# Kernel optimization log

Hardware: AMD Instinct MI355X
Metric: run time of the kernel (lower is better)

The kernel has to match this reference:

```python
import jax, jax.numpy as jnp
import numpy as np

EPS = 1e-8
LRELU_SLOPE = 0.2
ACT_GAIN = float(np.sqrt(2.0))  # def_gain for lrelu
GAIN = 1.0                      # forward default
CLAMP = 256.0


def setup_inputs() -> dict:
    key = jax.random.key(0)
    k1, k2 = jax.random.split(key)
    x = jax.random.normal(k1, (8, 128, 32, 32, 32), dtype=jnp.float32)
    weight = jax.random.normal(k2, (128, 128, 3, 3, 3), dtype=jnp.float32)
    bias = jnp.zeros((128,), dtype=jnp.float32)
    return {"x": x, "weight": weight, "bias": bias}


def _modulated_conv3d(x, weight, styles, padding, demodulate=True):
    # x: [B, Cin, D, H, W], weight: [Cout, Cin, kd, kh, kw], styles: [B, Cin]
    w = weight[None] * styles[:, None, :, None, None, None]  # [B, Cout, Cin, kd, kh, kw]
    if demodulate:
        dcoefs = jax.lax.rsqrt(jnp.sum(jnp.square(w), axis=(2, 3, 4, 5)) + EPS)  # [B, Cout]
        w = w * dcoefs[:, :, None, None, None, None]
    pad = [(padding, padding)] * 3

    def per_sample(xi, wi):
        # xi: [Cin, D, H, W], wi: [Cout, Cin, kd, kh, kw]
        return jax.lax.conv_general_dilated(
            xi[None], wi, window_strides=(1, 1, 1), padding=pad,
            dimension_numbers=("NCDHW", "OIDHW", "NCDHW"))[0]

    return jax.vmap(per_sample)(x, w)  # [B, Cout, D, H, W]


def reference(x, weight, bias):
    padding = weight.shape[-1] // 2
    styles = jnp.ones((x.shape[0], weight.shape[1]), dtype=x.dtype)
    y = _modulated_conv3d(x, weight, styles, padding)
    y = jax.nn.leaky_relu(y + bias[None, :, None, None, None], LRELU_SLOPE)
    # clamp_gain(act, act_gain*gain, 256*gain)
    return jnp.clip(y * (ACT_GAIN * GAIN), -CLAMP * GAIN, CLAMP * GAIN)
```

## Files before the change

kernel.cpp:

```cpp
#include <hip/hip_runtime.h>

typedef short bf16x8 __attribute__((ext_vector_type(8)));
typedef float f32x4  __attribute__((ext_vector_type(4)));

static __device__ __forceinline__ unsigned short f2bf(float f) {
    unsigned int u = __builtin_bit_cast(unsigned int, f);
    u += 0x7FFFu + ((u >> 16) & 1u);
    return (unsigned short)(u >> 16);
}

__global__ __launch_bounds__(256) void prep_w_k(const float* __restrict__ w,
                                                unsigned short* __restrict__ wn) {
    const int co = blockIdx.x;
    const int t  = threadIdx.x;
    const float* wc = w + co * 3456;
    float s = 0.f;
    for (int i = t; i < 3456; i += 256) { float v = wc[i]; s += v * v; }
#pragma unroll
    for (int off = 32; off; off >>= 1) s += __shfl_down(s, off);
    __shared__ float red[4];
    __shared__ float dsh;
    if ((t & 63) == 0) red[t >> 6] = s;
    __syncthreads();
    if (t == 0) dsh = rsqrtf(red[0] + red[1] + red[2] + red[3] + 1e-8f);
    __syncthreads();
    const float d = dsh;
    for (int i = t; i < 3456; i += 256) {
        int ci = i / 27, tap = i - ci * 27;
        float v = wc[i] * d;
        wn[((tap * 4 + (ci >> 5)) * 128 + co) * 32 + (ci & 31)] = f2bf(v);
    }
}

#define XSBASE 1280
__global__ __launch_bounds__(512, 2) void conv3d_k(
    const float* __restrict__ x, const unsigned short* __restrict__ wn,
    const float* __restrict__ bias, float* __restrict__ out) {
    __shared__ __align__(16) unsigned short lds[59200];

    const int t    = threadIdx.x;
    const int lane = t & 63;
    const int wid  = t >> 6;
    const int wr   = wid >> 1;
    const int wcn  = wid & 1;
    const int ll   = lane & 15;
    const int g    = lane >> 4;

    const int bid = blockIdx.x;
    const int b  = bid >> 6;
    const int dt = (bid >> 3) & 7, ht = bid & 7;
    const int d0 = dt * 4, h0 = ht * 4;

    const int sw  = t & 31;
    const int sg  = (t >> 5) & 3;
    const int rhi = t >> 7;
    const int bco = t >> 2, bgb = t & 3;

    f32x4 acc[8][4];
#pragma unroll
    for (int i = 0; i < 8; ++i)
#pragma unroll
        for (int j = 0; j < 4; ++j) acc[i][j] = (f32x4){0.f, 0.f, 0.f, 0.f};

    float bv[4][4];
#pragma unroll
    for (int nf = 0; nf < 4; ++nf) {
        f32x4 bb = *(const f32x4*)&bias[wcn * 64 + nf * 16 + g * 4];
#pragma unroll
        for (int q = 0; q < 4; ++q) bv[nf][q] = bb[q];
    }

    if (t < 288) {
        int pi  = t >> 2;
        int row = pi >> 1;
        int pos = row * 34 + (pi & 1) * 33;
        bf16x8 z = {0, 0, 0, 0, 0, 0, 0, 0};
        *(bf16x8*)&lds[(XSBASE + pos * 5 + (t & 3)) * 8] = z;
    }

    for (int c = 0; c < 4; ++c) {
        const int cibase = c * 32;
#pragma unroll
        for (int p = 0; p < 9; ++p) {
            int rowid = p * 4 + rhi;
            int pd = (rowid * 43) >> 8;
            int ph = rowid - pd * 6;
            int d = d0 - 1 + pd, h = h0 - 1 + ph;
            bool ok = ((unsigned)d < 32u) && ((unsigned)h < 32u);
            const float* src = x + (((b * 128 + cibase + sg * 8) * 32 + d) * 32 + h) * 32 + sw;
            float v[8];
#pragma unroll
            for (int j = 0; j < 8; ++j) v[j] = ok ? src[j * 32768] : 0.f;
            bf16x8 pk;
#pragma unroll
            for (int j = 0; j < 8; ++j) pk[j] = (short)f2bf(v[j]);
            int pos = (pd * 6 + ph) * 34 + sw + 1;
            *(bf16x8*)&lds[(XSBASE + pos * 5 + sg) * 8] = pk;
        }
        {
            bf16x8 bw = *(const bf16x8*)&wn[(0 * 4 + c) * 4096 + t * 8];
            *(bf16x8*)&lds[(bco * 5 + bgb) * 8] = bw;
        }
        __syncthreads();

#pragma unroll
        for (int tap = 0; tap < 27; ++tap) {
            const int od = tap / 9, oh = (tap / 3) % 3, ow = tap % 3;
            bf16x8 pref;
            if (tap < 26) pref = *(const bf16x8*)&wn[((tap + 1) * 4 + c) * 4096 + t * 8];

            const int bufo = (tap & 1) * 640;
            bf16x8 wf[4];
#pragma unroll
            for (int nf = 0; nf < 4; ++nf)
                wf[nf] = *(const bf16x8*)&lds[(bufo + (wcn * 64 + nf * 16 + ll) * 5 + g) * 8];

#pragma unroll
            for (int mf = 0; mf < 8; ++mf) {
                const int pd = wr + od;
                const int ph = (mf >> 1) + oh;
                const int wx = (mf & 1) * 16 + ll + ow;
                const int pos = (pd * 6 + ph) * 34 + wx;
                const bf16x8 xf = *(const bf16x8*)&lds[(XSBASE + pos * 5 + g) * 8];
#pragma unroll
                for (int nf = 0; nf < 4; ++nf)
                    acc[mf][nf] = __builtin_amdgcn_mfma_f32_16x16x32_bf16(
                        wf[nf], xf, acc[mf][nf], 0, 0, 0);
            }

            if (tap < 26)
                *(bf16x8*)&lds[(((tap + 1) & 1) * 640 + bco * 5 + bgb) * 8] = pref;
            __syncthreads();
        }
    }

    const int dd = d0 + wr;
#pragma unroll
    for (int mf = 0; mf < 8; ++mf) {
        const int hh = h0 + (mf >> 1);
        const int ww = (mf & 1) * 16 + ll;
#pragma unroll
        for (int nf = 0; nf < 4; ++nf) {
#pragma unroll
            for (int q = 0; q < 4; ++q) {
                const int co = wcn * 64 + nf * 16 + g * 4 + q;
                float v = acc[mf][nf][q] + bv[nf][q];
                v = v > 0.f ? v : v * 0.2f;
                v *= 1.41421356237f;
                v = fminf(fmaxf(v, -256.f), 256.f);
                out[(b * 128 + co) * 32768 + dd * 1024 + hh * 32 + ww] = v;
            }
        }
    }
}

extern "C" void kernel_launch(void* const* d_in, const int* in_sizes, int n_in,
                              void* d_out, int out_size, void* d_ws, size_t ws_size,
                              hipStream_t stream) {
    const float* x    = (const float*)d_in[0];
    const float* w    = (const float*)d_in[1];
    const float* bias = (const float*)d_in[2];
    float* out        = (float*)d_out;
    unsigned short* wn = (unsigned short*)d_ws;

    prep_w_k<<<128, 256, 0, stream>>>(w, wn);
    conv3d_k<<<512, 512, 0, stream>>>(x, wn, bias, out);
}
```

Before: 353.7 us.

## Load weights directly to registers, swizzle the input tile, stage output stores through LDS

Each wave now loads its weight fragments straight from global memory into registers and prefetches the next tap's fragments, instead of double-buffering them through LDS. This removes the per-tap __syncthreads barriers. The input tile is re-laid out with an XOR swizzle to reduce LDS bank conflicts. The epilogue writes activated results to LDS and then issues coalesced float4 global stores. The trade-offs are higher register pressure and repeated global/L2 weight reads per wave. The stride-33 float4 LDS reads may also be misaligned.

Measured after the change: 369.1 us. +4.4%, slower.

```diff
diff --git a/kernel.cpp b/kernel.cpp
--- a/kernel.cpp
+++ b/kernel.cpp
@@ -32,11 +32,12 @@
     }
 }
 
-#define XSBASE 1280
+#define NPOS 1224
 __global__ __launch_bounds__(512, 2) void conv3d_k(
     const float* __restrict__ x, const unsigned short* __restrict__ wn,
     const float* __restrict__ bias, float* __restrict__ out) {
-    __shared__ __align__(16) unsigned short lds[59200];
+    __shared__ __align__(16) unsigned short lds[NPOS * 32];
+    float* ldsf = reinterpret_cast<float*>(lds);
 
     const int t    = threadIdx.x;
     const int lane = t & 63;
@@ -54,7 +55,6 @@
     const int sw  = t & 31;
     const int sg  = (t >> 5) & 3;
     const int rhi = t >> 7;
-    const int bco = t >> 2, bgb = t & 3;
 
     f32x4 acc[8][4];
 #pragma unroll
@@ -75,10 +75,11 @@
         int row = pi >> 1;
         int pos = row * 34 + (pi & 1) * 33;
         bf16x8 z = {0, 0, 0, 0, 0, 0, 0, 0};
-        *(bf16x8*)&lds[(XSBASE + pos * 5 + (t & 3)) * 8] = z;
+        *(bf16x8*)&lds[pos * 32 + (t & 3) * 8] = z;
     }
 
     for (int c = 0; c < 4; ++c) {
+        if (c) __syncthreads();
         const int cibase = c * 32;
 #pragma unroll
         for (int p = 0; p < 9; ++p) {
@@ -94,62 +95,74 @@
             bf16x8 pk;
 #pragma unroll
             for (int j = 0; j < 8; ++j) pk[j] = (short)f2bf(v[j]);
-            int pos = (pd * 6 + ph) * 34 + sw + 1;
-            *(bf16x8*)&lds[(XSBASE + pos * 5 + sg) * 8] = pk;
-        }
-        {
-            bf16x8 bw = *(const bf16x8*)&wn[(0 * 4 + c) * 4096 + t * 8];
-            *(bf16x8*)&lds[(bco * 5 + bgb) * 8] = bw;
+            int pos = rowid * 34 + sw + 1;
+            int slot = sg ^ ((pos >> 1) & 3);
+            *(bf16x8*)&lds[pos * 32 + slot * 8] = pk;
         }
         __syncthreads();
+
+        const unsigned short* wbase = wn + (size_t)c * 4096 +
+                                      ((wcn * 64 + ll) * 32 + g * 8);
+        bf16x8 wf[4];
+#pragma unroll
+        for (int nf = 0; nf < 4; ++nf)
+            wf[nf] = *(const bf16x8*)&wbase[nf * 512];
 
 #pragma unroll
         for (int tap = 0; tap < 27; ++tap) {
             const int od = tap / 9, oh = (tap / 3) % 3, ow = tap % 3;
-            bf16x8 pref;
-            if (tap < 26) pref = *(const bf16x8*)&wn[((tap + 1) * 4 + c) * 4096 + t * 8];
-
-            const int bufo = (tap & 1) * 640;
-            bf16x8 wf[4];
+            bf16x8 wfn[4];
+            if (tap < 26) {
 #pragma unroll
-            for (int nf = 0; nf < 4; ++nf)
-                wf[nf] = *(const bf16x8*)&lds[(bufo + (wcn * 64 + nf * 16 + ll) * 5 + g) * 8];
-
+                for (int nf = 0; nf < 4; ++nf)
+                    wfn[nf] = *(const bf16x8*)&wbase[(tap + 1) * 16384 + nf * 512];
+            }
 #pragma unroll
             for (int mf = 0; mf < 8; ++mf) {
                 const int pd = wr + od;
                 const int ph = (mf >> 1) + oh;
                 const int wx = (mf & 1) * 16 + ll + ow;
                 const int pos = (pd * 6 + ph) * 34 + wx;
-                const bf16x8 xf = *(const bf16x8*)&lds[(XSBASE + pos * 5 + g) * 8];
+                const int slot = g ^ ((pos >> 1) & 3);
+                const bf16x8 xf = *(const bf16x8*)&lds[pos * 32 + slot * 8];
 #pragma unroll
                 for (int nf = 0; nf < 4; ++nf)
                     acc[mf][nf] = __builtin_amdgcn_mfma_f32_16x16x32_bf16(
                         wf[nf], xf, acc[mf][nf], 0, 0, 0);
             }
-
-            if (tap < 26)
-                *(bf16x8*)&lds[(((tap + 1) & 1) * 640 + bco * 5 + bgb) * 8] = pref;
-            __syncthreads();
+#pragma unroll
+            for (int nf = 0; nf < 4; ++nf) wf[nf] = wfn[nf];
         }
     }
 
-    const int dd = d0 + wr;
 #pragma unroll
-    for (int mf = 0; mf < 8; ++mf) {
-        const int hh = h0 + (mf >> 1);
-        const int ww = (mf & 1) * 16 + ll;
+    for (int h = 0; h < 4; ++h) {
+        __syncthreads();
 #pragma unroll
-        for (int nf = 0; nf < 4; ++nf) {
+        for (int whalf = 0; whalf < 2; ++whalf) {
+            const int mf = h * 2 + whalf;
 #pragma unroll
-            for (int q = 0; q < 4; ++q) {
-                const int co = wcn * 64 + nf * 16 + g * 4 + q;
-                float v = acc[mf][nf][q] + bv[nf][q];
-                v = v > 0.f ? v : v * 0.2f;
-                v *= 1.41421356237f;
-                v = fminf(fmaxf(v, -256.f), 256.f);
-                out[(b * 128 + co) * 32768 + dd * 1024 + hh * 32 + ww] = v;
+            for (int nf = 0; nf < 4; ++nf) {
+#pragma unroll
+                for (int q = 0; q < 4; ++q) {
+                    const int co = wcn * 64 + nf * 16 + g * 4 + q;
+                    float v = acc[mf][nf][q] + bv[nf][q];
+                    v = v > 0.f ? v : v * 0.2f;
+                    v *= 1.41421356237f;
+                    v = fminf(fmaxf(v, -256.f), 256.f);
+                    ldsf[(co * 4 + wr) * 33 + whalf * 16 + ll] = v;
+                }
             }
+        }
+        __syncthreads();
+#pragma unroll
+        for (int it = 0; it < 8; ++it) {
+            const int row = it * 64 + (t >> 3);
+            const int ls  = t & 7;
+            f32x4 v = *(f32x4*)&ldsf[row * 33 + ls * 4];
+            const int co = row >> 2, wr2 = row & 3;
+            *(f32x4*)&out[(size_t)(b * 128 + co) * 32768 +
+                          (d0 + wr2) * 1024 + (h0 + h) * 32 + ls * 4] = v;
         }
     }
 }
```
